# Performance work log

Hardware: AMD Instinct MI355X
Metric: run time of the kernel (lower is better)

Reference implementation:

```python
import jax, jax.numpy as jnp
import numpy as np
from jax import lax

NUM_LAYERS = 3
NUM_QUBITS = 8
BATCH = 131072
DIM = 2 ** NUM_QUBITS  # 256


def _rot_mats(params):
    # params: (L, Q, 3) angles for RX, RY, RZ. Returns combined U = RZ @ RY @ RX, (L, Q, 2, 2) complex64.
    half = params * 0.5
    cx = jnp.cos(half[..., 0]).astype(jnp.complex64)
    sx = jnp.sin(half[..., 0]).astype(jnp.complex64)
    cy = jnp.cos(half[..., 1]).astype(jnp.complex64)
    sy = jnp.sin(half[..., 1]).astype(jnp.complex64)
    ezm = jnp.exp(-1j * half[..., 2]).astype(jnp.complex64)
    ezp = jnp.exp(1j * half[..., 2]).astype(jnp.complex64)
    zero = jnp.zeros_like(cx)
    RX = jnp.stack([jnp.stack([cx, -1j * sx], -1), jnp.stack([-1j * sx, cx], -1)], -2)
    RY = jnp.stack([jnp.stack([cy, -sy], -1), jnp.stack([sy, cy], -1)], -2)
    RZ = jnp.stack([jnp.stack([ezm, zero], -1), jnp.stack([zero, ezp], -1)], -2)
    return jnp.einsum('lqij,lqjk,lqkm->lqim', RZ, RY, RX)


def _apply_1q(state, U, wire):
    # state: (B, 2,2,...,2); wire w lives on axis w+1 (PennyLane wire 0 = most significant bit)
    ax = wire + 1
    return jnp.moveaxis(jnp.tensordot(U, state, axes=((1,), (ax,))), 0, ax)


def _apply_cnot(state, ctrl, tgt):
    c_ax, t_ax = ctrl + 1, tgt + 1
    s0 = lax.index_in_dim(state, 0, axis=c_ax, keepdims=True)
    s1 = lax.index_in_dim(state, 1, axis=c_ax, keepdims=True)
    s1 = jnp.flip(s1, axis=t_ax)
    return jnp.concatenate([s0, s1], axis=c_ax)


def _circuit(params, state_re, state_im):
    U = _rot_mats(params)  # (L, Q, 2, 2)
    state = (state_re + 1j * state_im).astype(jnp.complex64)
    state = state.reshape((state.shape[0],) + (2,) * NUM_QUBITS)
    for l in range(NUM_LAYERS):
        for q in range(NUM_QUBITS):
            state = _apply_1q(state, U[l, q], q)
        for q in range(NUM_QUBITS):
            state = _apply_cnot(state, q, (q + 1) % NUM_QUBITS)
    state = state.reshape(state.shape[0], DIM)
    # probability that wire 0 measures |0>: sum |amp|^2 over first half of amplitudes
    half = state[:, : DIM // 2]
    return jnp.sum(half.real ** 2 + half.imag ** 2, axis=1).astype(jnp.float32)


def setup_inputs() -> dict:
    key = jax.random.key(0)
    k1, k2, k3 = jax.random.split(key, 3)
    params = jax.random.uniform(k1, (NUM_LAYERS, NUM_QUBITS, 3), dtype=jnp.float32)
    sr = jax.random.normal(k2, (BATCH, DIM), dtype=jnp.float32)
    si = jax.random.normal(k3, (BATCH, DIM), dtype=jnp.float32)
    norm = jnp.sqrt(jnp.sum(sr ** 2 + si ** 2, axis=1, keepdims=True))
    return {"params": params, "state_re": sr / norm, "state_im": si / norm}


def reference(params, state_re, state_im):
    return _circuit(params, state_re, state_im)
```

## Files before the change

kernel.cpp:

```cpp
#include <hip/hip_runtime.h>
#include <stdint.h>

#define NLAYERS 3
#define NQ 8
#define DIM 256
#define KDIM 512
#define BM 64
#define AST 520
#define NBLK (131072 / BM)

typedef float  f32x4  __attribute__((ext_vector_type(4)));
typedef __bf16 bf16x8 __attribute__((ext_vector_type(8)));

__device__ __forceinline__ unsigned short f2bf(float f){
    union { float f; uint32_t u; } v; v.f = f;
    uint32_t u = v.u;
    u += 0x7fffu + ((u >> 16) & 1u);
    return (unsigned short)(u >> 16);
}

__device__ __forceinline__ float2 cmul(float2 a, float2 b){
    return make_float2(a.x*b.x - a.y*b.y, a.x*b.y + a.y*b.x);
}

__global__ __launch_bounds__(256) void build_g_kernel(const float* __restrict__ params,
                                                      unsigned short* __restrict__ G){
    __shared__ float2 st[2][DIM];
    __shared__ float2 gm[NLAYERS*NQ][4];
    const int j = blockIdx.x;
    const int i = threadIdx.x;

    if (i < NLAYERS*NQ){
        const float* pp = params + i*3;
        float hx = 0.5f*pp[0], hy = 0.5f*pp[1], hz = 0.5f*pp[2];
        float cx = cosf(hx), sx = sinf(hx);
        float cy = cosf(hy), sy = sinf(hy);
        float cz = cosf(hz), sz = sinf(hz);
        float2 ezm = make_float2(cz, -sz), ezp = make_float2(cz, sz);
        float2 m00 = make_float2( cy*cx,  sy*sx);
        float2 m01 = make_float2(-sy*cx, -cy*sx);
        float2 m10 = make_float2( sy*cx, -cy*sx);
        float2 m11 = make_float2( cy*cx, -sy*sx);
        gm[i][0] = cmul(ezm, m00);
        gm[i][1] = cmul(ezm, m01);
        gm[i][2] = cmul(ezp, m10);
        gm[i][3] = cmul(ezp, m11);
    }

    int psrc = i;
    #pragma unroll
    for (int q = NQ-1; q >= 0; --q){
        int c  = 7 - q;
        int tb = 7 - ((q + 1) & 7);
        psrc = ((psrc >> c) & 1) ? (psrc ^ (1 << tb)) : psrc;
    }

    int cur = 0;
    st[0][i] = make_float2(i == j ? 1.0f : 0.0f, 0.0f);
    __syncthreads();

    for (int l = 0; l < NLAYERS; ++l){
        for (int q = 0; q < NQ; ++q){
            float2 U0a = gm[l*NQ+q][0], U0b = gm[l*NQ+q][1];
            float2 U1a = gm[l*NQ+q][2], U1b = gm[l*NQ+q][3];
            int p  = 7 - q;
            int bs = (i >> p) & 1;
            int i0 = i & ~(1 << p), i1 = i | (1 << p);
            float2 a0 = st[cur][i0], a1 = st[cur][i1];
            float2 ua = bs ? U1a : U0a;
            float2 ub = bs ? U1b : U0b;
            float2 r;
            r.x = ua.x*a0.x - ua.y*a0.y + ub.x*a1.x - ub.y*a1.y;
            r.y = ua.x*a0.y + ua.y*a0.x + ub.x*a1.y + ub.y*a1.x;
            st[cur ^ 1][i] = r;
            cur ^= 1;
            __syncthreads();
        }
        float2 r = st[cur][psrc];
        st[cur ^ 1][i] = r;
        cur ^= 1;
        __syncthreads();
    }

    const int m = i & 127;
    float2 a = st[cur][m];
    unsigned short lo, hi;
    if (i < 128){ lo = f2bf(a.x); hi = f2bf(-a.y); }
    else        { lo = f2bf(a.y); hi = f2bf( a.x); }
    G[(size_t)i*KDIM + j]        = lo;
    G[(size_t)i*KDIM + j + DIM]  = hi;
}

__global__ __launch_bounds__(256, 2) void qform_kernel(const float* __restrict__ sr,
                                                       const float* __restrict__ si,
                                                       const unsigned short* __restrict__ G,
                                                       float* __restrict__ out){
    __shared__ unsigned short As[BM * AST];
    __shared__ float red[4 * BM];

    const int tid  = threadIdx.x;
    const int lane = tid & 63;
    const int w    = tid >> 6;
    const int l15  = lane & 15;
    const int quad = lane >> 4;
    const size_t mbase = (size_t)blockIdx.x * BM;

    {
        const int r  = tid >> 2;
        const int cs = (tid & 3) * 64;
        #pragma unroll
        for (int h = 0; h < 2; ++h){
            const float* gp = (h ? si : sr) + (mbase + r)*DIM + cs;
            unsigned short* dst = &As[r*AST + h*256 + cs];
            #pragma unroll
            for (int o = 0; o < 8; ++o){
                float4 fa = ((const float4*)gp)[o*2];
                float4 fb = ((const float4*)gp)[o*2+1];
                uint4 pk;
                pk.x = f2bf(fa.x) | ((uint32_t)f2bf(fa.y) << 16);
                pk.y = f2bf(fa.z) | ((uint32_t)f2bf(fa.w) << 16);
                pk.z = f2bf(fb.x) | ((uint32_t)f2bf(fb.y) << 16);
                pk.w = f2bf(fb.z) | ((uint32_t)f2bf(fb.w) << 16);
                *(uint4*)(dst + o*8) = pk;
            }
        }
    }

    f32x4 acc[4][4];
    const f32x4 vzero = {0.0f, 0.0f, 0.0f, 0.0f};
    #pragma unroll
    for (int ii = 0; ii < 4; ++ii)
        #pragma unroll
        for (int jj = 0; jj < 4; ++jj)
            acc[ii][jj] = vzero;

    const unsigned short* gB = G + ((size_t)(w*64 + l15))*KDIM + quad*8;

    __syncthreads();

    #pragma unroll 4
    for (int ks = 0; ks < 16; ++ks){
        bf16x8 a[4], b[4];
        #pragma unroll
        for (int jj = 0; jj < 4; ++jj)
            b[jj] = *(const bf16x8*)(gB + (size_t)jj*16*KDIM + ks*32);
        #pragma unroll
        for (int ii = 0; ii < 4; ++ii)
            a[ii] = *(const bf16x8*)&As[(ii*16 + l15)*AST + ks*32 + quad*8];
        #pragma unroll
        for (int ii = 0; ii < 4; ++ii)
            #pragma unroll
            for (int jj = 0; jj < 4; ++jj)
                acc[ii][jj] = __builtin_amdgcn_mfma_f32_16x16x32_bf16(
                    a[ii], b[jj], acc[ii][jj], 0, 0, 0);
    }

    float s[4][4];
    #pragma unroll
    for (int ii = 0; ii < 4; ++ii)
        #pragma unroll
        for (int r = 0; r < 4; ++r){
            float t = 0.0f;
            #pragma unroll
            for (int jj = 0; jj < 4; ++jj){ float v = acc[ii][jj][r]; t += v*v; }
            s[ii][r] = t;
        }
    #pragma unroll
    for (int ii = 0; ii < 4; ++ii)
        #pragma unroll
        for (int r = 0; r < 4; ++r){
            float t = s[ii][r];
            t += __shfl_xor(t, 1);
            t += __shfl_xor(t, 2);
            t += __shfl_xor(t, 4);
            t += __shfl_xor(t, 8);
            s[ii][r] = t;
        }
    if (l15 == 0){
        #pragma unroll
        for (int ii = 0; ii < 4; ++ii)
            #pragma unroll
            for (int r = 0; r < 4; ++r)
                red[w*64 + ii*16 + quad*4 + r] = s[ii][r];
    }
    __syncthreads();
    if (tid < 64){
        float o = red[tid] + red[64 + tid] + red[128 + tid] + red[192 + tid];
        out[mbase + tid] = o;
    }
}

extern "C" void kernel_launch(void* const* d_in, const int* in_sizes, int n_in,
                              void* d_out, int out_size, void* d_ws, size_t ws_size,
                              hipStream_t stream){
    const float* params = (const float*)d_in[0];
    const float* sr     = (const float*)d_in[1];
    const float* si     = (const float*)d_in[2];
    unsigned short* G   = (unsigned short*)d_ws;
    float* out          = (float*)d_out;

    build_g_kernel<<<dim3(DIM), dim3(256), 0, stream>>>(params, G);
    qform_kernel<<<dim3(NBLK), dim3(256), 0, stream>>>(sr, si, G, out);
}
```

Baseline: 336.3 us.

## Persist G in registers and software-pipeline A loads across row chunks

The qform kernel now launches a fixed grid of 512-thread blocks. Each block loops over four 64-row chunks and keeps its slice of the G matrix resident in registers instead of reloading it from global memory on every k-step. The real and imaginary input halves are double-buffered in LDS, so global loads for the next half or chunk are issued while MFMAs run on the current one. This targets repeated G traffic and exposed load latency, at the cost of much higher register pressure (32 uint4 per thread) that may limit occupancy under launch bounds of 512x2.

```diff
diff --git a/kernel.cpp b/kernel.cpp
--- a/kernel.cpp
+++ b/kernel.cpp
@@ -5,9 +5,9 @@
 #define NQ 8
 #define DIM 256
 #define KDIM 512
-#define BM 64
-#define AST 520
-#define NBLK (131072 / BM)
+#define CCHUNKS 4
+#define GRID 512
+#define AST 264
 
 typedef float  f32x4  __attribute__((ext_vector_type(4)));
 typedef __bf16 bf16x8 __attribute__((ext_vector_type(8)));
@@ -91,102 +91,126 @@
     G[(size_t)i*KDIM + j + DIM]  = hi;
 }
 
-__global__ __launch_bounds__(256, 2) void qform_kernel(const float* __restrict__ sr,
+__global__ __launch_bounds__(512, 2) void qform_kernel(const float* __restrict__ sr,
                                                        const float* __restrict__ si,
                                                        const unsigned short* __restrict__ G,
                                                        float* __restrict__ out){
-    __shared__ unsigned short As[BM * AST];
-    __shared__ float red[4 * BM];
+    __shared__ unsigned short As[2][64][AST];
+    __shared__ float red[8][64];
 
     const int tid  = threadIdx.x;
     const int lane = tid & 63;
     const int w    = tid >> 6;
     const int l15  = lane & 15;
     const int quad = lane >> 4;
-    const size_t mbase = (size_t)blockIdx.x * BM;
-
+    const int arow = tid >> 3;
+    const int sub  = tid & 7;
+    const size_t mblock = (size_t)blockIdx.x * (CCHUNKS*64);
+
+    float4 L[8];
     {
-        const int r  = tid >> 2;
-        const int cs = (tid & 3) * 64;
-        #pragma unroll
-        for (int h = 0; h < 2; ++h){
-            const float* gp = (h ? si : sr) + (mbase + r)*DIM + cs;
-            unsigned short* dst = &As[r*AST + h*256 + cs];
+        const float* gp = sr + (mblock + arow)*DIM + sub*8;
+        #pragma unroll
+        for (int o = 0; o < 4; ++o){
+            L[2*o]   = *(const float4*)(gp + o*64);
+            L[2*o+1] = *(const float4*)(gp + o*64 + 4);
+        }
+    }
+
+    uint4 Breg[2][16];
+    {
+        const unsigned short* gB = G + (size_t)(w*32 + l15)*KDIM + quad*8;
+        #pragma unroll
+        for (int jj = 0; jj < 2; ++jj)
             #pragma unroll
-            for (int o = 0; o < 8; ++o){
-                float4 fa = ((const float4*)gp)[o*2];
-                float4 fb = ((const float4*)gp)[o*2+1];
-                uint4 pk;
-                pk.x = f2bf(fa.x) | ((uint32_t)f2bf(fa.y) << 16);
-                pk.y = f2bf(fa.z) | ((uint32_t)f2bf(fa.w) << 16);
-                pk.z = f2bf(fb.x) | ((uint32_t)f2bf(fb.y) << 16);
-                pk.w = f2bf(fb.z) | ((uint32_t)f2bf(fb.w) << 16);
-                *(uint4*)(dst + o*8) = pk;
-            }
-        }
-    }
-
-    f32x4 acc[4][4];
+            for (int kg = 0; kg < 16; ++kg)
+                Breg[jj][kg] = *(const uint4*)(gB + (size_t)jj*16*KDIM + kg*32);
+    }
+
+    f32x4 acc[4][2];
     const f32x4 vzero = {0.0f, 0.0f, 0.0f, 0.0f};
     #pragma unroll
-    for (int ii = 0; ii < 4; ++ii)
-        #pragma unroll
-        for (int jj = 0; jj < 4; ++jj)
-            acc[ii][jj] = vzero;
-
-    const unsigned short* gB = G + ((size_t)(w*64 + l15))*KDIM + quad*8;
-
+    for (int ii = 0; ii < 4; ++ii){ acc[ii][0] = vzero; acc[ii][1] = vzero; }
+
+    #define WRITE_A(buf)                                                        \
+        {                                                                       \
+            unsigned short* dst = &As[buf][arow][0];                            \
+            _Pragma("unroll")                                                   \
+            for (int o = 0; o < 4; ++o){                                        \
+                float4 f0 = L[2*o], f1 = L[2*o+1];                              \
+                uint4 pk;                                                       \
+                pk.x = f2bf(f0.x) | ((uint32_t)f2bf(f0.y) << 16);               \
+                pk.y = f2bf(f0.z) | ((uint32_t)f2bf(f0.w) << 16);               \
+                pk.z = f2bf(f1.x) | ((uint32_t)f2bf(f1.y) << 16);               \
+                pk.w = f2bf(f1.z) | ((uint32_t)f2bf(f1.w) << 16);               \
+                *(uint4*)(dst + sub*8 + o*64) = pk;                             \
+            }                                                                   \
+        }
+
+    #define ISSUE_A(Z, c)                                                       \
+        {                                                                       \
+            const float* gp = (Z) + (mblock + (c)*64 + arow)*DIM + sub*8;       \
+            _Pragma("unroll")                                                   \
+            for (int o = 0; o < 4; ++o){                                        \
+                L[2*o]   = *(const float4*)(gp + o*64);                         \
+                L[2*o+1] = *(const float4*)(gp + o*64 + 4);                     \
+            }                                                                   \
+        }
+
+    #define COMPUTE8(buf, h)                                                    \
+        {                                                                       \
+            _Pragma("unroll")                                                   \
+            for (int ks = 0; ks < 8; ++ks){                                     \
+                bf16x8 a[4];                                                    \
+                _Pragma("unroll")                                               \
+                for (int ii = 0; ii < 4; ++ii)                                  \
+                    a[ii] = *(const bf16x8*)&As[buf][ii*16 + l15][ks*32 + quad*8];\
+                _Pragma("unroll")                                               \
+                for (int ii = 0; ii < 4; ++ii)                                  \
+                    _Pragma("unroll")                                           \
+                    for (int jj = 0; jj < 2; ++jj){                             \
+                        union { uint4 u; bf16x8 f; } bb;                        \
+                        bb.u = Breg[jj][(h)*8 + ks];                            \
+                        acc[ii][jj] = __builtin_amdgcn_mfma_f32_16x16x32_bf16(  \
+                            a[ii], bb.f, acc[ii][jj], 0, 0, 0);                 \
+                    }                                                           \
+            }                                                                   \
+        }
+
+    WRITE_A(0);
     __syncthreads();
-
-    #pragma unroll 4
-    for (int ks = 0; ks < 16; ++ks){
-        bf16x8 a[4], b[4];
-        #pragma unroll
-        for (int jj = 0; jj < 4; ++jj)
-            b[jj] = *(const bf16x8*)(gB + (size_t)jj*16*KDIM + ks*32);
-        #pragma unroll
-        for (int ii = 0; ii < 4; ++ii)
-            a[ii] = *(const bf16x8*)&As[(ii*16 + l15)*AST + ks*32 + quad*8];
+    ISSUE_A(si, 0);
+
+    for (int c = 0; c < CCHUNKS; ++c){
+        COMPUTE8(0, 0);
+        WRITE_A(1);
+        __syncthreads();
+        if (c + 1 < CCHUNKS) ISSUE_A(sr, c+1);
+        COMPUTE8(1, 1);
+
         #pragma unroll
         for (int ii = 0; ii < 4; ++ii)
             #pragma unroll
-            for (int jj = 0; jj < 4; ++jj)
-                acc[ii][jj] = __builtin_amdgcn_mfma_f32_16x16x32_bf16(
-                    a[ii], b[jj], acc[ii][jj], 0, 0, 0);
-    }
-
-    float s[4][4];
-    #pragma unroll
-    for (int ii = 0; ii < 4; ++ii)
-        #pragma unroll
-        for (int r = 0; r < 4; ++r){
-            float t = 0.0f;
-            #pragma unroll
-            for (int jj = 0; jj < 4; ++jj){ float v = acc[ii][jj][r]; t += v*v; }
-            s[ii][r] = t;
-        }
-    #pragma unroll
-    for (int ii = 0; ii < 4; ++ii)
-        #pragma unroll
-        for (int r = 0; r < 4; ++r){
-            float t = s[ii][r];
-            t += __shfl_xor(t, 1);
-            t += __shfl_xor(t, 2);
-            t += __shfl_xor(t, 4);
-            t += __shfl_xor(t, 8);
-            s[ii][r] = t;
-        }
-    if (l15 == 0){
-        #pragma unroll
-        for (int ii = 0; ii < 4; ++ii)
-            #pragma unroll
-            for (int r = 0; r < 4; ++r)
-                red[w*64 + ii*16 + quad*4 + r] = s[ii][r];
-    }
-    __syncthreads();
-    if (tid < 64){
-        float o = red[tid] + red[64 + tid] + red[128 + tid] + red[192 + tid];
-        out[mbase + tid] = o;
+            for (int r = 0; r < 4; ++r){
+                float v0 = acc[ii][0][r], v1 = acc[ii][1][r];
+                float t = v0*v0 + v1*v1;
+                t += __shfl_xor(t, 1);
+                t += __shfl_xor(t, 2);
+                t += __shfl_xor(t, 4);
+                t += __shfl_xor(t, 8);
+                if (l15 == 0) red[w][ii*16 + quad*4 + r] = t;
+            }
+        #pragma unroll
+        for (int ii = 0; ii < 4; ++ii){ acc[ii][0] = vzero; acc[ii][1] = vzero; }
+
+        if (c + 1 < CCHUNKS) WRITE_A(0);
+        __syncthreads();
+        if (tid < 64){
+            float o = red[0][tid] + red[1][tid] + red[2][tid] + red[3][tid]
+                    + red[4][tid] + red[5][tid] + red[6][tid] + red[7][tid];
+            out[mblock + c*64 + tid] = o;
+        }
+        if (c + 1 < CCHUNKS) ISSUE_A(si, c+1);
     }
 }
 
@@ -200,5 +224,5 @@
     float* out          = (float*)d_out;
 
     build_g_kernel<<<dim3(DIM), dim3(256), 0, stream>>>(params, G);
-    qform_kernel<<<dim3(NBLK), dim3(256), 0, stream>>>(sr, si, G, out);
-}
+    qform_kernel<<<dim3(GRID), dim3(512), 0, stream>>>(sr, si, G, out);
+}
```

Measured after the change: 296.4 us. -11.9%, faster.

## Halve row tile and double-buffer A staging across K chunks

Applied to the files above, without the earlier changes.

Shrinks the per-block row tile from 64 to 32 and replaces the up-front conversion of the whole A tile with a K-chunked double-buffered pipeline. Global loads for the next chunk are issued before the current chunk's MFMAs and written to LDS afterward. The smaller LDS footprint allows four blocks per CU instead of two. The cost is a barrier per chunk and G (B operand) being reloaded twice as often per output row.

```diff
diff --git a/kernel.cpp b/kernel.cpp
--- a/kernel.cpp
+++ b/kernel.cpp
@@ -5,9 +5,9 @@
 #define NQ 8
 #define DIM 256
 #define KDIM 512
-#define BM 64
-#define AST 520
+#define BM 32
 #define NBLK (131072 / BM)
+#define AST 72
 
 typedef float  f32x4  __attribute__((ext_vector_type(4)));
 typedef __bf16 bf16x8 __attribute__((ext_vector_type(8)));
@@ -91,103 +91,103 @@
     G[(size_t)i*KDIM + j + DIM]  = hi;
 }
 
-__global__ __launch_bounds__(256, 2) void qform_kernel(const float* __restrict__ sr,
+__global__ __launch_bounds__(256, 4) void qform_kernel(const float* __restrict__ sr,
                                                        const float* __restrict__ si,
                                                        const unsigned short* __restrict__ G,
                                                        float* __restrict__ out){
-    __shared__ unsigned short As[BM * AST];
-    __shared__ float red[4 * BM];
+    __shared__ unsigned short As[2][BM * AST];
+    __shared__ float red[4][BM];
 
     const int tid  = threadIdx.x;
     const int lane = tid & 63;
     const int w    = tid >> 6;
     const int l15  = lane & 15;
     const int quad = lane >> 4;
+    const int srow = tid >> 3;
+    const int sseg = tid & 7;
     const size_t mbase = (size_t)blockIdx.x * BM;
 
-    {
-        const int r  = tid >> 2;
-        const int cs = (tid & 3) * 64;
-        #pragma unroll
-        for (int h = 0; h < 2; ++h){
-            const float* gp = (h ? si : sr) + (mbase + r)*DIM + cs;
-            unsigned short* dst = &As[r*AST + h*256 + cs];
-            #pragma unroll
-            for (int o = 0; o < 8; ++o){
-                float4 fa = ((const float4*)gp)[o*2];
-                float4 fb = ((const float4*)gp)[o*2+1];
-                uint4 pk;
-                pk.x = f2bf(fa.x) | ((uint32_t)f2bf(fa.y) << 16);
-                pk.y = f2bf(fa.z) | ((uint32_t)f2bf(fa.w) << 16);
-                pk.z = f2bf(fb.x) | ((uint32_t)f2bf(fb.y) << 16);
-                pk.w = f2bf(fb.z) | ((uint32_t)f2bf(fb.w) << 16);
-                *(uint4*)(dst + o*8) = pk;
-            }
-        }
-    }
-
-    f32x4 acc[4][4];
+    float4 L0, L1;
+
+    #define ISSUE_A(kc1)                                                       \
+        {                                                                      \
+            const float* gp = (((kc1) < 4) ? sr : si)                          \
+                + (mbase + srow)*(size_t)DIM + (((kc1) & 3)*64 + sseg*8);      \
+            L0 = ((const float4*)gp)[0];                                       \
+            L1 = ((const float4*)gp)[1];                                       \
+        }
+
+    #define WRITE_A(buf)                                                       \
+        {                                                                      \
+            uint4 pk;                                                          \
+            pk.x = f2bf(L0.x) | ((uint32_t)f2bf(L0.y) << 16);                  \
+            pk.y = f2bf(L0.z) | ((uint32_t)f2bf(L0.w) << 16);                  \
+            pk.z = f2bf(L1.x) | ((uint32_t)f2bf(L1.y) << 16);                  \
+            pk.w = f2bf(L1.z) | ((uint32_t)f2bf(L1.w) << 16);                  \
+            *(uint4*)&As[buf][srow*AST + sseg*8] = pk;                         \
+        }
+
+    ISSUE_A(0);
+    WRITE_A(0);
+
+    f32x4 acc[2][4];
     const f32x4 vzero = {0.0f, 0.0f, 0.0f, 0.0f};
     #pragma unroll
-    for (int ii = 0; ii < 4; ++ii)
+    for (int ii = 0; ii < 2; ++ii)
         #pragma unroll
         for (int jj = 0; jj < 4; ++jj)
             acc[ii][jj] = vzero;
 
-    const unsigned short* gB = G + ((size_t)(w*64 + l15))*KDIM + quad*8;
+    const unsigned short* gB = G + (size_t)(w*64 + l15)*KDIM + quad*8;
 
     __syncthreads();
 
-    #pragma unroll 4
-    for (int ks = 0; ks < 16; ++ks){
-        bf16x8 a[4], b[4];
+    for (int kc = 0; kc < 8; ++kc){
+        if (kc < 7) ISSUE_A(kc + 1);
+
+        const int buf = kc & 1;
         #pragma unroll
-        for (int jj = 0; jj < 4; ++jj)
-            b[jj] = *(const bf16x8*)(gB + (size_t)jj*16*KDIM + ks*32);
-        #pragma unroll
-        for (int ii = 0; ii < 4; ++ii)
-            a[ii] = *(const bf16x8*)&As[(ii*16 + l15)*AST + ks*32 + quad*8];
-        #pragma unroll
-        for (int ii = 0; ii < 4; ++ii)
+        for (int ks = 0; ks < 2; ++ks){
+            bf16x8 a[2], b[4];
             #pragma unroll
             for (int jj = 0; jj < 4; ++jj)
-                acc[ii][jj] = __builtin_amdgcn_mfma_f32_16x16x32_bf16(
-                    a[ii], b[jj], acc[ii][jj], 0, 0, 0);
-    }
-
-    float s[4][4];
+                b[jj] = *(const bf16x8*)(gB + (size_t)jj*16*KDIM + kc*64 + ks*32);
+            #pragma unroll
+            for (int ii = 0; ii < 2; ++ii)
+                a[ii] = *(const bf16x8*)&As[buf][(ii*16 + l15)*AST + ks*32 + quad*8];
+            #pragma unroll
+            for (int ii = 0; ii < 2; ++ii)
+                #pragma unroll
+                for (int jj = 0; jj < 4; ++jj)
+                    acc[ii][jj] = __builtin_amdgcn_mfma_f32_16x16x32_bf16(
+                        a[ii], b[jj], acc[ii][jj], 0, 0, 0);
+        }
+
+        if (kc < 7) WRITE_A((kc + 1) & 1);
+        __syncthreads();
+    }
+
     #pragma unroll
-    for (int ii = 0; ii < 4; ++ii)
+    for (int ii = 0; ii < 2; ++ii)
         #pragma unroll
         for (int r = 0; r < 4; ++r){
             float t = 0.0f;
             #pragma unroll
             for (int jj = 0; jj < 4; ++jj){ float v = acc[ii][jj][r]; t += v*v; }
-            s[ii][r] = t;
-        }
-    #pragma unroll
-    for (int ii = 0; ii < 4; ++ii)
-        #pragma unroll
-        for (int r = 0; r < 4; ++r){
-            float t = s[ii][r];
             t += __shfl_xor(t, 1);
             t += __shfl_xor(t, 2);
             t += __shfl_xor(t, 4);
             t += __shfl_xor(t, 8);
-            s[ii][r] = t;
-        }
-    if (l15 == 0){
-        #pragma unroll
-        for (int ii = 0; ii < 4; ++ii)
-            #pragma unroll
-            for (int r = 0; r < 4; ++r)
-                red[w*64 + ii*16 + quad*4 + r] = s[ii][r];
-    }
+            if (l15 == 0) red[w][ii*16 + quad*4 + r] = t;
+        }
     __syncthreads();
-    if (tid < 64){
-        float o = red[tid] + red[64 + tid] + red[128 + tid] + red[192 + tid];
+    if (tid < BM){
+        float o = red[0][tid] + red[1][tid] + red[2][tid] + red[3][tid];
         out[mbase + tid] = o;
     }
+
+    #undef ISSUE_A
+    #undef WRITE_A
 }
 
 extern "C" void kernel_launch(void* const* d_in, const int* in_sizes, int n_in,
```

New measurement: 339.2 us. No clear change (+0.9%).
